# Optimization experiments

Hardware: AMD Instinct MI355X
Metric: run time of the kernel (lower is better)

The kernel has to match this reference:

```python
import jax, jax.numpy as jnp
import numpy as np

N, E, EL = 50000, 150000, 300000   # atoms, bonds(=line-graph nodes), line-graph edges
FN, FE, FX = 128, 128, 64          # atom, bond, angle feature dims (encode_dim)
H, D = 4, 64                        # num_heads, per-head hidden
SLOPE = 0.01                        # torch leaky_relu default


def _leaky(x):
    return jnp.where(x >= 0, x, SLOPE * x)


def _seg_softmax(logits, seg, n):
    # softmax over edges grouped by destination (DGL edge_softmax). logits [E, H]
    m = jax.ops.segment_max(logits, seg, num_segments=n)
    ex = jnp.exp(logits - m[seg])
    s = jax.ops.segment_sum(ex, seg, num_segments=n)
    return ex / s[seg]


def _seg_mean(x, seg, n):
    # mean of incoming edge feats per dst node; empty segments -> 0 (DGL behavior)
    s = jax.ops.segment_sum(x, seg, num_segments=n)
    c = jax.ops.segment_sum(jnp.ones((x.shape[0], 1), x.dtype), seg, num_segments=n)
    return s / jnp.maximum(c, 1.0)


def setup_inputs() -> dict:
    key = jax.random.key(0)
    ks = iter(jax.random.split(key, 40))
    nrm = lambda shape, sc=0.1: jax.random.normal(next(ks), shape, jnp.float32) * sc
    z = lambda n: jnp.zeros((n,), jnp.float32)
    inp = {
        'nfeats': nrm((N, FN), 1.0),
        'efeats': nrm((E, FE), 1.0),
        'xfeats': nrm((EL, FX), 1.0),
        # EGAT layer (atom graph)
        'e_Wni': nrm((H * D, FN)), 'e_Wnj': nrm((H * D, FN)), 'e_Wfij': nrm((H * D, FE)),
        'e_Wnode': nrm((H * D, FN + FE)), 'e_bnode': z(H * D),
        'e_attn': nrm((H, D)), 'e_bias': z(H * D),
        # Path_Complex line-graph branch
        'lg_Wni': nrm((H * D, D)), 'lg_Wnj': nrm((H * D, D)), 'lg_Wfij': nrm((H * D, FX)),
        'lg_Wnode': nrm((H * D, D + FX)), 'lg_bnode': z(H * D),
        'lg_attn': nrm((H, D)), 'lg_bias': z(H * D),
        # Path_Complex graph branch
        'g_Wni': nrm((H * D, D)), 'g_Wnj': nrm((H * D, D)), 'g_Wfij': nrm((H * D, D)),
        'g_Wnode': nrm((H * D, D + D)), 'g_bnode': z(H * D),
        'g_attn': nrm((H, D)), 'g_bias': z(H * D),
        # graph / line-graph connectivity
        'src': jax.random.randint(next(ks), (E,), 0, N, jnp.int32),
        'dst': jax.random.randint(next(ks), (E,), 0, N, jnp.int32),
        'lsrc': jax.random.randint(next(ks), (EL,), 0, E, jnp.int32),
        'ldst': jax.random.randint(next(ks), (EL,), 0, E, jnp.int32),
    }
    return inp


def _forward(nfeats, efeats, xfeats,
             e_Wni, e_Wnj, e_Wfij, e_Wnode, e_bnode, e_attn, e_bias,
             lg_Wni, lg_Wnj, lg_Wfij, lg_Wnode, lg_bnode, lg_attn, lg_bias,
             g_Wni, g_Wnj, g_Wfij, g_Wnode, g_bnode, g_attn, g_bias,
             src, dst, lsrc, ldst):
    # ---- EGAT layer on atom graph ----
    fo = _leaky((nfeats @ e_Wni.T)[src] + (nfeats @ e_Wnj.T)[dst] + efeats @ e_Wfij.T + e_bias)
    fov = fo.reshape(E, H, D)
    e_att = _seg_softmax((fov * e_attn[None]).sum(-1), dst, N)      # [E, H]
    agg = _seg_mean(efeats, dst, N)                                   # [N, FE]
    h = (jnp.concatenate([nfeats, agg], 1) @ e_Wnode.T + e_bnode).reshape(N, H, D)
    h_node = _leaky(jax.ops.segment_sum(h[src] * e_att[:, :, None], dst, num_segments=N)).sum(1)
    f_edge = fov.sum(1)                                               # [E, D]

    # ---- Path_Complex layer: line-graph (bond->angle) branch ----
    lgf = _leaky((f_edge @ lg_Wni.T)[lsrc] + (f_edge @ lg_Wnj.T)[ldst] + xfeats @ lg_Wfij.T + lg_bias)
    lgv = lgf.reshape(EL, H, D)
    a_lg = _seg_softmax((lgv * lg_attn[None]).sum(-1), ldst, E)      # [EL, H]
    aggx = _seg_mean(xfeats, ldst, E)                                 # [E, FX]
    m1 = (jnp.concatenate([f_edge, aggx], 1) @ lg_Wnode.T + lg_bnode).reshape(E, H, D)
    lg_h = _leaky(jax.ops.segment_sum(m1[lsrc] * a_lg[:, :, None], ldst, num_segments=E)).sum(1)

    # ---- Path_Complex layer: graph (atom->bond) branch ----
    gf = _leaky((h_node @ g_Wni.T)[src] + (h_node @ g_Wnj.T)[dst] + f_edge @ g_Wfij.T + g_bias)
    gv = gf.reshape(E, H, D)
    a_g = _seg_softmax((gv * g_attn[None]).sum(-1), dst, N)          # [E, H] -> l_graph ndata 'a'
    node_edge = h_node[src] + h_node[dst]
    m2 = (jnp.concatenate([node_edge, f_edge], 1) @ g_Wnode.T + g_bnode).reshape(E, H, D)
    # u_mul_v on line graph: message = h_out[lsrc] * a[ldst]
    g_h = _leaky(jax.ops.segment_sum(m2[lsrc] * a_g[ldst][:, :, None], ldst, num_segments=E)).sum(1)

    return g_h + lg_h                                                 # [E, D] updated bond feats


def reference(nfeats, efeats, xfeats,
              e_Wni, e_Wnj, e_Wfij, e_Wnode, e_bnode, e_attn, e_bias,
              lg_Wni, lg_Wnj, lg_Wfij, lg_Wnode, lg_bnode, lg_attn, lg_bias,
              g_Wni, g_Wnj, g_Wfij, g_Wnode, g_bnode, g_attn, g_bias,
              src, dst, lsrc, ldst):
    return _forward(nfeats, efeats, xfeats,
                    e_Wni, e_Wnj, e_Wfij, e_Wnode, e_bnode, e_attn, e_bias,
                    lg_Wni, lg_Wnj, lg_Wfij, lg_Wnode, lg_bnode, lg_attn, lg_bias,
                    g_Wni, g_Wnj, g_Wfij, g_Wnode, g_bnode, g_attn, g_bias,
                    src, dst, lsrc, ldst)
```

## Files before the change

### kernel.cpp

```cpp
#include <hip/hip_runtime.h>
#include <hip/hip_bf16.h>
#include <math.h>

typedef __hip_bfloat16 bf16;
typedef short bf16x8 __attribute__((ext_vector_type(8)));
typedef short s16x4 __attribute__((ext_vector_type(4)));
typedef float f32x4 __attribute__((ext_vector_type(4)));

__device__ __forceinline__ float b2f(bf16 x) { return __bfloat162float(x); }
__device__ __forceinline__ bf16  f2b(float x) { return __float2bfloat16(x); }
__device__ __forceinline__ float leaky(float x) { return x >= 0.0f ? x : 0.01f * x; }
__device__ __forceinline__ float sb2f(short s) {
  return __uint_as_float(((unsigned)(unsigned short)s) << 16);
}
__device__ __forceinline__ short f2bs(float x) {
  unsigned u = __float_as_uint(x);
  u += 0x7FFFu + ((u >> 16) & 1u);
  return (short)(u >> 16);
}
__device__ __forceinline__ float ldF(const void* p, size_t i, int f) {
  return f ? ((const float*)p)[i] : b2f(((const bf16*)p)[i]);
}
__device__ __forceinline__ bf16x8 ldA8(const char* row, int k, int f) {
  if (!f) return *(const bf16x8*)(row + (size_t)k * 2);
  const float4* p = (const float4*)(row + (size_t)k * 4);
  float4 a = p[0], b = p[1];
  bf16x8 r;
  r[0] = f2bs(a.x); r[1] = f2bs(a.y); r[2] = f2bs(a.z); r[3] = f2bs(a.w);
  r[4] = f2bs(b.x); r[5] = f2bs(b.y); r[6] = f2bs(b.z); r[7] = f2bs(b.w);
  return r;
}

__global__ void k_detect(const unsigned* __restrict__ w, int* __restrict__ flag) {
  __shared__ int cnt[256];
  unsigned x = w[threadIdx.x];
  unsigned ex = (x >> 7) & 0xFFu;
  cnt[threadIdx.x] = (ex >= 96u && ex <= 144u) ? 1 : 0;
  __syncthreads();
  for (int s = 128; s > 0; s >>= 1) {
    if (threadIdx.x < s) cnt[threadIdx.x] += cnt[threadIdx.x + s];
    __syncthreads();
  }
  if (threadIdx.x == 0) *flag = (cnt[0] < 128) ? 1 : 0;
}

struct WArgs { const void* src[21]; int beg[22]; int len[21]; };
__global__ void k_cvt_all(WArgs wa, bf16* __restrict__ dst, int total,
                          const int* __restrict__ flagp) {
  int f = *flagp;
  for (int i = blockIdx.x * 256 + threadIdx.x; i < total; i += gridDim.x * 256) {
    int t = 0;
    while (t < 20 && i >= wa.beg[t + 1]) ++t;
    int loc = i - wa.beg[t];
    bf16 v = f2b(0.0f);
    if (loc < wa.len[t])
      v = f ? f2b(((const float*)wa.src[t])[loc]) : ((const bf16*)wa.src[t])[loc];
    dst[i] = v;
  }
}

__global__ void k_cvt2(const float* __restrict__ a, bf16* __restrict__ da, size_t na,
                       const float* __restrict__ c, bf16* __restrict__ dc, size_t nc,
                       const int* __restrict__ flagp) {
  if (!*flagp) return;
  size_t tot = (na + nc) >> 2;
  for (size_t i = (size_t)blockIdx.x * 256 + threadIdx.x; i < tot;
       i += (size_t)gridDim.x * 256) {
    size_t j = i << 2;
    const float* s; bf16* d; size_t loc;
    if (j < na) { s = a; d = da; loc = j; }
    else        { s = c; d = dc; loc = j - na; }
    float4 v = *(const float4*)(s + loc);
    s16x4 o; o[0] = f2bs(v.x); o[1] = f2bs(v.y); o[2] = f2bs(v.z); o[3] = f2bs(v.w);
    *(s16x4*)(d + loc) = o;
  }
}

__global__ void k_izero(int* __restrict__ p, int n) {
  int i = blockIdx.x * 256 + threadIdx.x;
  for (; i < n; i += gridDim.x * 256) p[i] = 0;
}

__global__ void k_hist(const int* __restrict__ seg, int* __restrict__ deg, int n) {
  int i = blockIdx.x * 256 + threadIdx.x;
  if (i < n) atomicAdd(&deg[seg[i]], 1);
}

__global__ __launch_bounds__(256)
void k_scan_local(const int* __restrict__ deg, int* __restrict__ rp,
                  int* __restrict__ bsum, int n) {
  __shared__ int sh[256];
  int tid = threadIdx.x;
  int base = blockIdx.x * 4096 + tid * 16;
  int v[16]; int s = 0;
#pragma unroll
  for (int j = 0; j < 16; ++j) { v[j] = (base + j < n) ? deg[base + j] : 0; s += v[j]; }
  sh[tid] = s;
  __syncthreads();
  for (int o = 1; o < 256; o <<= 1) {
    int t = (tid >= o) ? sh[tid - o] : 0;
    __syncthreads();
    sh[tid] += t;
    __syncthreads();
  }
  int run = sh[tid] - s;
#pragma unroll
  for (int j = 0; j < 16; ++j) {
    run += v[j];
    if (base + j < n) rp[base + j + 1] = run;
  }
  if (tid == 255) bsum[blockIdx.x] = sh[255];
  if (blockIdx.x == 0 && tid == 0) rp[0] = 0;
}
__global__ __launch_bounds__(256)
void k_scan_bsum(int* __restrict__ bsum, int nb) {
  __shared__ int sh[256];
  __shared__ int carry;
  int tid = threadIdx.x;
  if (tid == 0) carry = 0;
  __syncthreads();
  for (int base = 0; base < nb; base += 256) {
    int i = base + tid;
    int v = (i < nb) ? bsum[i] : 0;
    sh[tid] = v;
    __syncthreads();
    for (int o = 1; o < 256; o <<= 1) {
      int t = (tid >= o) ? sh[tid - o] : 0;
      __syncthreads();
      sh[tid] += t;
      __syncthreads();
    }
    if (i < nb) bsum[i] = carry + sh[tid] - v;
    int tot = sh[255];
    __syncthreads();
    if (tid == 0) carry += tot;
    __syncthreads();
  }
}
__global__ __launch_bounds__(256)
void k_scan_add(int* __restrict__ rp, const int* __restrict__ bsum, int n) {
  int b = blockIdx.x + 1;
  int ofs = bsum[b];
  int base = b * 4096 + threadIdx.x * 16;
#pragma unroll
  for (int j = 0; j < 16; ++j) {
    int idx = base + j + 1;
    if (idx <= n) rp[idx] += ofs;
  }
}

__global__ void k_slot(const int* __restrict__ seg, const int* __restrict__ rp,
                       int* __restrict__ cur, int* __restrict__ eid,
                       const int* __restrict__ aux1, int* __restrict__ av1,
                       int* __restrict__ pos, int n) {
  int i = blockIdx.x * 256 + threadIdx.x;
  if (i >= n) return;
  int t = seg[i];
  int p = atomicAdd(&cur[t], 1);
  int j = rp[t] + p;
  eid[j] = i;
  if (av1) av1[j] = aux1[i];
  if (pos) pos[i] = j;
}

__global__ void k_gmean(const void* __restrict__ X, const void* __restrict__ Xc, int mode,
                        const int* __restrict__ rp, const int* __restrict__ eid,
                        bf16* __restrict__ out, int n, int width,
                        const int* __restrict__ flagp) {
  int f = (mode == 2) ? *flagp : mode;
  if (Xc && f) { X = Xc; f = 0; }
  int d = threadIdx.x;
  int row = blockIdx.x * blockDim.y + threadIdx.y;
  if (row >= n) return;
  int b = rp[row], e = rp[row + 1];
  float s = 0.0f;
  for (int j = b; j < e; ++j) s += ldF(X, (size_t)eid[j] * width + d, f);
  out[(size_t)row * width + d] = f2b(s / fmaxf((float)(e - b), 1.0f));
}

__global__ __launch_bounds__(256)
void k_mgemm(const void* __restrict__ A0, const void* __restrict__ A0c, int m0mode, int K0,
             const void* __restrict__ A1, int m1mode, int Ktot,
             const bf16* __restrict__ W, int whs, const bf16* __restrict__ bias,
             bf16* __restrict__ C, int cs, int M,
             const int* __restrict__ flagp) {
  int tid = threadIdx.x;
  int w = tid >> 6, lane = tid & 63, l15 = lane & 15, q = lane >> 4;
  int h = blockIdx.y;
  int fl = *flagp;
  int f0 = (m0mode == 2) ? fl : m0mode;
  if (A0c && f0) { A0 = A0c; f0 = 0; }
  int f1 = (m1mode == 2) ? fl : m1mode;
  const bf16* Wh = W + (size_t)h * whs;
  int colofs = h * 64;
  int m0 = blockIdx.x * 64 + w * 16;
  int mA = m0 + l15; if (mA > M - 1) mA = M - 1;
  const char* rowA0 = (const char*)A0 + (size_t)mA * K0 * (f0 ? 4 : 2);
  const char* rowA1 = A1 ? (const char*)A1 + (size_t)mA * (Ktot - K0) * (f1 ? 4 : 2) : nullptr;

  f32x4 acc[4] = {{0,0,0,0},{0,0,0,0},{0,0,0,0},{0,0,0,0}};
  for (int k = q * 8; k < Ktot; k += 32) {
    bf16x8 a;
    if (k < K0) a = ldA8(rowA0, k, f0);
    else        a = ldA8(rowA1, k - K0, f1);
    const bf16* wb = Wh + (size_t)l15 * Ktot + k;
#pragma unroll
    for (int t = 0; t < 4; ++t)
      acc[t] = __builtin_amdgcn_mfma_f32_16x16x32_bf16(
          a, *(const bf16x8*)(wb + (size_t)(t * 16) * Ktot), acc[t], 0, 0, 0);
  }
#pragma unroll
  for (int t = 0; t < 4; ++t) {
    int col = t * 16 + l15;
    float bv = bias ? b2f(bias[colofs + col]) : 0.0f;
#pragma unroll
    for (int r = 0; r < 4; ++r) {
      int m = m0 + q * 4 + r;
      if (m < M) C[(size_t)m * cs + colofs + col] = f2b(acc[t][r] + bv);
    }
  }
}

__global__ __launch_bounds__(256)
void k_mgemm2sw(const void* __restrict__ A, const void* __restrict__ Ac, int mode, int K,
                const bf16* __restrict__ W1, const bf16* __restrict__ W2, int whs,
                int h0, int HB, bf16* __restrict__ C1, bf16* __restrict__ C2, int M,
                const int* __restrict__ flagp) {
  int tid = threadIdx.x;
  int w = tid >> 6, lane = tid & 63, l15 = lane & 15, q = lane >> 4;
  int hy = blockIdx.y;
  int h = h0 + hy;
  int f = (mode == 2) ? *flagp : mode;
  if (Ac && f) { A = Ac; f = 0; }
  const bf16* W1h = W1 + (size_t)h * whs;
  const bf16* W2h = W2 + (size_t)h * whs;
  int cs = HB * 64;
  int m0 = blockIdx.x * 64 + w * 16;
  int mA = m0 + l15; if (mA > M - 1) mA = M - 1;
  const char* rowA = (const char*)A + (size_t)mA * K * (f ? 4 : 2);

  f32x4 a1[4] = {{0,0,0,0},{0,0,0,0},{0,0,0,0},{0,0,0,0}};
  f32x4 a2[4] = {{0,0,0,0},{0,0,0,0},{0,0,0,0},{0,0,0,0}};
  for (int k = q * 8; k < K; k += 32) {
    bf16x8 a = ldA8(rowA, k, f);
    const bf16* w1 = W1h + (size_t)l15 * K + k;
    const bf16* w2 = W2h + (size_t)l15 * K + k;
#pragma unroll
    for (int t = 0; t < 4; ++t) {
      a1[t] = __builtin_amdgcn_mfma_f32_16x16x32_bf16(
          a, *(const bf16x8*)(w1 + (size_t)(t * 16) * K), a1[t], 0, 0, 0);
      a2[t] = __builtin_amdgcn_mfma_f32_16x16x32_bf16(
          a, *(const bf16x8*)(w2 + (size_t)(t * 16) * K), a2[t], 0, 0, 0);
    }
  }
  int ofs = l15 * 4 * HB + hy * 4;
#pragma unroll
  for (int r = 0; r < 4; ++r) {
    int m = m0 + q * 4 + r;
    if (m < M) {
      s16x4 o1, o2;
#pragma unroll
      for (int t = 0; t < 4; ++t) { o1[t] = f2bs(a1[t][r]); o2[t] = f2bs(a2[t][r]); }
      *(s16x4*)(C1 + (size_t)m * cs + ofs) = o1;
      *(s16x4*)(C2 + (size_t)m * cs + ofs) = o2;
    }
  }
}

template<int NK>
__global__ __launch_bounds__(256)
void k_mcomb4sw(const void* __restrict__ A, const void* __restrict__ Ac, int mode,
                const bf16* __restrict__ W, int whs,
                const bf16* __restrict__ bias, const bf16* __restrict__ attn,
                const bf16* __restrict__ G1, const bf16* __restrict__ G2,
                const int* __restrict__ gi, const int* __restrict__ gj,
                const int* __restrict__ posw,
                float* __restrict__ lg4, bf16* __restrict__ fout,
                int M, const int* __restrict__ flagp) {
  constexpr int K = NK * 32;
  int tid = threadIdx.x;
  int w = tid >> 6, lane = tid & 63, l15 = lane & 15, q = lane >> 4;
  int f = (mode == 2) ? *flagp : mode;
  if (Ac && f) { A = Ac; f = 0; }
  int m0 = blockIdx.x * 64 + w * 16;
  int mA = m0 + l15; if (mA > M - 1) mA = M - 1;
  const char* rowA = (const char*)A + (size_t)mA * K * (f ? 4 : 2);
  bf16x8 af[NK];
#pragma unroll
  for (int i = 0; i < NK; ++i) af[i] = ldA8(rowA, q * 8 + 32 * i, f);
  int pIdx[4]; bool okr[4];
  bf16x8 gv1[4][2], gv2[4][2];
#pragma unroll
  for (int r = 0; r < 4; ++r) {
    int m = m0 + q * 4 + r;
    okr[r] = m < M; int mc = okr[r] ? m : M - 1;
    pIdx[r] = posw ? posw[mc] : mc;
    const bf16* p1 = G1 + (size_t)gi[mc] * 256 + l15 * 16;
    const bf16* p2 = G2 + (size_t)gj[mc] * 256 + l15 * 16;
    gv1[r][0] = *(const bf16x8*)p1; gv1[r][1] = *(const bf16x8*)(p1 + 8);
    gv2[r][0] = *(const bf16x8*)p2; gv2[r][1] = *(const bf16x8*)(p2 + 8);
  }
  f32x4 fs[4] = {{0,0,0,0},{0,0,0,0},{0,0,0,0},{0,0,0,0}};
#pragma unroll
  for (int h = 0; h < 4; ++h) {
    const bf16* Wh = W + (size_t)h * whs;
    f32x4 acc[4] = {{0,0,0,0},{0,0,0,0},{0,0,0,0},{0,0,0,0}};
#pragma unroll
    for (int i = 0; i < NK; ++i) {
      const bf16* wb = Wh + (size_t)l15 * K + q * 8 + 32 * i;
#pragma unroll
      for (int t = 0; t < 4; ++t)
        acc[t] = __builtin_amdgcn_mfma_f32_16x16x32_bf16(
            af[i], *(const bf16x8*)(wb + (size_t)(t * 16) * K), acc[t], 0, 0, 0);
    }
    float bv[4], av[4];
#pragma unroll
    for (int t = 0; t < 4; ++t) {
      bv[t] = b2f(bias[h * 64 + t * 16 + l15]);
      av[t] = b2f(attn[h * 64 + t * 16 + l15]);
    }
    float part[4];
#pragma unroll
    for (int r = 0; r < 4; ++r) {
      float p = 0.0f;
#pragma unroll
      for (int t = 0; t < 4; ++t) {
        float v = acc[t][r] + bv[t] + sb2f(gv1[r][h >> 1][(h & 1) * 4 + t])
                                    + sb2f(gv2[r][h >> 1][(h & 1) * 4 + t]);
        v = leaky(v);
        p += v * av[t];
        fs[t][r] += v;
      }
      part[r] = p;
    }
#pragma unroll
    for (int o = 1; o < 16; o <<= 1)
#pragma unroll
      for (int r = 0; r < 4; ++r) part[r] += __shfl_xor(part[r], o, 64);
    if (l15 == 0) {
#pragma unroll
      for (int r = 0; r < 4; ++r)
        if (okr[r]) lg4[(size_t)pIdx[r] * 4 + h] = part[r];
    }
  }
  if (fout) {
#pragma unroll
    for (int t = 0; t < 4; ++t) {
      int col = t * 16 + l15;
#pragma unroll
      for (int r = 0; r < 4; ++r)
        if (okr[r]) fout[(size_t)(m0 + q * 4 + r) * 64 + col] = f2b(fs[t][r]);
    }
  }
}

template<int NK>
__global__ __launch_bounds__(256)
void k_mcomb2h(const void* __restrict__ A, const void* __restrict__ Ac, int mode,
               const bf16* __restrict__ W, int whs, int h0,
               const bf16* __restrict__ bias, const bf16* __restrict__ attn,
               const bf16* __restrict__ G1, const bf16* __restrict__ G2,
               const int* __restrict__ gi, const int* __restrict__ gj,
               const int* __restrict__ posw,
               float* __restrict__ lg4, int M, const int* __restrict__ flagp) {
  constexpr int K = NK * 32;
  int tid = threadIdx.x;
  int w = tid >> 6, lane = tid & 63, l15 = lane & 15, q = lane >> 4;
  int f = (mode == 2) ? *flagp : mode;
  if (Ac && f) { A = Ac; f = 0; }
  int m0 = blockIdx.x * 64 + w * 16;
  int mA = m0 + l15; if (mA > M - 1) mA = M - 1;
  const char* rowA = (const char*)A + (size_t)mA * K * (f ? 4 : 2);
  bf16x8 af[NK];
#pragma unroll
  for (int i = 0; i < NK; ++i) af[i] = ldA8(rowA, q * 8 + 32 * i, f);
  int pIdx[4]; bool okr[4];
  bf16x8 gv1[4], gv2[4];
#pragma unroll
  for (int r = 0; r < 4; ++r) {
    int m = m0 + q * 4 + r;
    okr[r] = m < M; int mc = okr[r] ? m : M - 1;
    pIdx[r] = posw ? posw[mc] : mc;
    gv1[r] = *(const bf16x8*)(G1 + (size_t)gi[mc] * 128 + l15 * 8);
    gv2[r] = *(const bf16x8*)(G2 + (size_t)gj[mc] * 128 + l15 * 8);
  }
#pragma unroll
  for (int hy = 0; hy < 2; ++hy) {
    int h = h0 + hy;
    const bf16* Wh = W + (size_t)h * whs;
    f32x4 acc[4] = {{0,0,0,0},{0,0,0,0},{0,0,0,0},{0,0,0,0}};
#pragma unroll
    for (int i = 0; i < NK; ++i) {
      const bf16* wb = Wh + (size_t)l15 * K + q * 8 + 32 * i;
#pragma unroll
      for (int t = 0; t < 4; ++t)
        acc[t] = __builtin_amdgcn_mfma_f32_16x16x32_bf16(
            af[i], *(const bf16x8*)(wb + (size_t)(t * 16) * K), acc[t], 0, 0, 0);
    }
    float bv[4], av[4];
#pragma unroll
    for (int t = 0; t < 4; ++t) {
      bv[t] = b2f(bias[h * 64 + t * 16 + l15]);
      av[t] = b2f(attn[h * 64 + t * 16 + l15]);
    }
    float part[4];
#pragma unroll
    for (int r = 0; r < 4; ++r) {
      float p = 0.0f;
#pragma unroll
      for (int t = 0; t < 4; ++t) {
        float v = acc[t][r] + bv[t] + sb2f(gv1[r][hy * 4 + t]) + sb2f(gv2[r][hy * 4 + t]);
        p += leaky(v) * av[t];
      }
      part[r] = p;
    }
#pragma unroll
    for (int o = 1; o < 16; o <<= 1)
#pragma unroll
      for (int r = 0; r < 4; ++r) part[r] += __shfl_xor(part[r], o, 64);
    if (l15 == 0) {
#pragma unroll
      for (int r = 0; r < 4; ++r)
        if (okr[r]) lg4[(size_t)pIdx[r] * 4 + h] = part[r];
    }
  }
}

__global__ __launch_bounds__(256)
void k_smax4_csr(float* __restrict__ lg, const int* __restrict__ rp, int n) {
  int tid = blockIdx.x * 256 + threadIdx.x;
  int row = tid >> 2, h = tid & 3;
  if (row >= n) return;
  int b = rp[row], e = rp[row + 1];
  float m = -INFINITY;
  for (int j = b; j < e; ++j) m = fmaxf(m, lg[(size_t)j * 4 + h]);
  float s = 0.0f;
  for (int j = b; j < e; ++j) {
    float ex = expf(lg[(size_t)j * 4 + h] - m);
    lg[(size_t)j * 4 + h] = ex;
    s += ex;
  }
  float inv = 1.0f / s;
  for (int j = b; j < e; ++j) lg[(size_t)j * 4 + h] *= inv;
}
__global__ __launch_bounds__(256)
void k_smax4_eid(float* __restrict__ lg, const int* __restrict__ rp,
                 const int* __restrict__ eid, int n) {
  int tid = blockIdx.x * 256 + threadIdx.x;
  int row = tid >> 2, h = tid & 3;
  if (row >= n) return;
  int b = rp[row], e = rp[row + 1];
  float m = -INFINITY;
  for (int j = b; j < e; ++j) m = fmaxf(m, lg[(size_t)eid[j] * 4 + h]);
  float s = 0.0f;
  for (int j = b; j < e; ++j) {
    float ex = expf(lg[(size_t)eid[j] * 4 + h] - m);
    lg[(size_t)eid[j] * 4 + h] = ex;
    s += ex;
  }
  float inv = 1.0f / s;
  for (int j = b; j < e; ++j) lg[(size_t)eid[j] * 4 + h] *= inv;
}

__global__ __launch_bounds__(256)
void k_ghnode(const bf16* __restrict__ H, const float* __restrict__ lg4c,
              const int* __restrict__ rp, const int* __restrict__ srcv,
              bf16* __restrict__ hnode, int N) {
  int d = threadIdx.x, h = threadIdx.y;
  int n = blockIdx.x;
  int b = rp[n], e = rp[n + 1];
  float s = 0.0f;
  for (int j = b; j < e; ++j)
    s += b2f(H[(size_t)srcv[j] * 256 + h * 64 + d]) * lg4c[(size_t)j * 4 + h];
  float v = leaky(s);
  __shared__ float sh[4][64];
  if (h > 0) sh[h][d] = v;
  __syncthreads();
  if (h == 0)
    hnode[(size_t)n * 64 + d] = f2b(v + sh[1][d] + sh[2][d] + sh[3][d]);
}

__global__ void k_gout2(const bf16* __restrict__ M1, const float* __restrict__ lgE4,
                        int h, const int* __restrict__ rp, const int* __restrict__ lsv,
                        float* __restrict__ out, int E, int first) {
  int d = threadIdx.x;
  int t = blockIdx.x * 4 + threadIdx.y;
  if (t >= E) return;
  int b = rp[t], e = rp[t + 1];
  float s = 0.0f;
  for (int j = b; j < e; ++j)
    s += b2f(M1[(size_t)lsv[j] * 64 + d]) * lgE4[(size_t)j * 4 + h];
  float val = leaky(s);
  if (first) out[(size_t)t * 64 + d] = val;
  else       out[(size_t)t * 64 + d] += val;
}

__global__ void k_gout3(const bf16* __restrict__ M2, const float* __restrict__ lg4n,
                        const int* __restrict__ rp, const int* __restrict__ lsv,
                        float* __restrict__ out, int E, int h) {
  int d = threadIdx.x;
  int t = blockIdx.x * 4 + threadIdx.y;
  if (t >= E) return;
  int b = rp[t], e = rp[t + 1];
  float s = 0.0f;
  for (int j = b; j < e; ++j) s += b2f(M2[(size_t)lsv[j] * 64 + d]);
  float a = lg4n[(size_t)t * 4 + h];
  out[(size_t)t * 64 + d] += leaky(a * s);
}

__global__ void k_addpair(const bf16* __restrict__ hn, const int* __restrict__ src,
                          const int* __restrict__ dst, bf16* __restrict__ ne, int E) {
  int d = threadIdx.x;
  int e = blockIdx.x * 4 + threadIdx.y;
  if (e >= E) return;
  ne[(size_t)e * 64 + d] =
      f2b(b2f(hn[(size_t)src[e] * 64 + d]) + b2f(hn[(size_t)dst[e] * 64 + d]));
}

__global__ void k_cast(void* __restrict__ out, const float* __restrict__ a, size_t n,
                       const int* __restrict__ flagp) {
  int f = *flagp;
  size_t i = (size_t)blockIdx.x * blockDim.x + threadIdx.x;
  size_t st = (size_t)gridDim.x * blockDim.x;
  for (; i < n; i += st) {
    if (f) ((float*)out)[i] = a[i];
    else   ((bf16*)out)[i] = f2b(a[i]);
  }
}

extern "C" void kernel_launch(void* const* d_in, const int* in_sizes, int n_in,
                              void* d_out, int out_size, void* d_ws, size_t ws_size,
                              hipStream_t stream) {
  const int* src  = (const int*)d_in[24];
  const int* dst  = (const int*)d_in[25];
  const int* lsrc = (const int*)d_in[26];
  const int* ldst = (const int*)d_in[27];

  const int N  = in_sizes[0] / 128;
  const int E  = in_sizes[24];
  const int EL = in_sizes[26];
  (void)n_in; (void)out_size; (void)ws_size;

  char* base = (char*)d_ws;
  size_t off = 0;
  auto alloc = [&](size_t bytes) -> char* {
    char* p = base + off;
    off = (off + bytes + 255) & ~(size_t)255;
    return p;
  };
  int* flag = (int*)alloc(256);
  size_t wofs[28]; size_t wtot = 0;
  for (int i = 3; i <= 23; ++i) { wofs[i] = wtot; wtot += (size_t)((in_sizes[i] + 127) & ~127); }
  bf16* WA = (bf16*)alloc(wtot * 2);

  int*   tmpi  = (int*)alloc((size_t)2 * E * 4);
  int*   rpN   = (int*)alloc((size_t)(N + 1) * 4);
  int*   eidN  = (int*)alloc((size_t)E * 4);
  int*   srcv  = (int*)alloc((size_t)E * 4);
  int*   posN  = (int*)alloc((size_t)E * 4);
  int*   rpE   = (int*)alloc((size_t)(E + 1) * 4);
  int*   eidEL = (int*)alloc((size_t)EL * 4);
  int*   lsv   = (int*)alloc((size_t)EL * 4);
  int*   posE  = (int*)alloc((size_t)EL * 4);
  int*   bsum  = (int*)alloc(((size_t)((E > N ? E : N) + 4095) / 4096 + 8) * 4);
  bf16*  fedge = (bf16*)alloc((size_t)E * 64 * 2);
  bf16*  hnode = (bf16*)alloc((size_t)N * 64 * 2);
  float* outacc= (float*)alloc((size_t)E * 64 * 4);
  bf16*  aggB  = (bf16*)alloc((size_t)E * 64 * 2);
  size_t saElems = (size_t)E * 128 > (size_t)N * 256 ? (size_t)E * 128 : (size_t)N * 256;
  bf16*  SA    = (bf16*)alloc(saElems * 2);
  float* logE4 = (float*)alloc((size_t)E * 4 * 4);
  float* logEL4= (float*)alloc((size_t)EL * 4 * 4);
  bf16*  nb    = (bf16*)alloc((size_t)N * 128 * 2);

  bf16* SBo = (bf16*)outacc;
  bf16* xb  = (bf16*)d_out;

  dim3 blk(256);
  const unsigned tN = (N + 63) / 64, tEg = (E + 63) / 64, tELg = (EL + 63) / 64;
  const unsigned gE4 = (E + 3) / 4;
  const unsigned cE = (E + 255) / 256, cEL = (EL + 255) / 256;
  const int nbN = (N + 4095) / 4096, nbE = (E + 4095) / 4096;

  k_detect<<<dim3(1), blk, 0, stream>>>((const unsigned*)d_in[0], flag);
  WArgs wa;
  for (int i = 3; i <= 23; ++i) {
    wa.src[i - 3] = d_in[i];
    wa.beg[i - 3] = (int)wofs[i];
    wa.len[i - 3] = in_sizes[i];
  }
  wa.beg[21] = (int)wtot;
  k_cvt_all<<<dim3(512), blk, 0, stream>>>(wa, WA, (int)wtot, flag);
  k_cvt2<<<dim3(2048), blk, 0, stream>>>(
      (const float*)d_in[0], nb, (size_t)N * 128,
      (const float*)d_in[2], xb, (size_t)EL * 64, flag);

  int* deg = tmpi; int* cur = tmpi + E;
  k_izero<<<dim3(1024), blk, 0, stream>>>(tmpi, 2 * E);
  k_hist<<<dim3(cE), blk, 0, stream>>>(dst, deg, E);
  k_scan_local<<<dim3(nbN), blk, 0, stream>>>(deg, rpN, bsum, N);
  k_scan_bsum<<<dim3(1), blk, 0, stream>>>(bsum, nbN);
  if (nbN > 1) k_scan_add<<<dim3(nbN - 1), blk, 0, stream>>>(rpN, bsum, N);
  k_slot<<<dim3(cE), blk, 0, stream>>>(dst, rpN, cur, eidN, src, srcv, posN, E);
  k_izero<<<dim3(1024), blk, 0, stream>>>(tmpi, 2 * E);
  k_hist<<<dim3(cEL), blk, 0, stream>>>(ldst, deg, EL);
  k_scan_local<<<dim3(nbE), blk, 0, stream>>>(deg, rpE, bsum, E);
  k_scan_bsum<<<dim3(1), blk, 0, stream>>>(bsum, nbE);
  if (nbE > 1) k_scan_add<<<dim3(nbE - 1), blk, 0, stream>>>(rpE, bsum, E);
  k_slot<<<dim3(cEL), blk, 0, stream>>>(ldst, rpE, cur, eidEL, lsrc, lsv, posE, EL);

  k_gmean<<<dim3((N + 1) / 2), dim3(128, 2), 0, stream>>>(d_in[1], nullptr, 2, rpN, eidN,
                                                          aggB, N, 128, flag);
  k_mgemm2sw<<<dim3(tN, 4), blk, 0, stream>>>(d_in[0], nb, 2, 128,
      WA + wofs[3], WA + wofs[4], 8192, 0, 4, SA, SBo, N, flag);
  k_mcomb4sw<4><<<dim3(tEg), blk, 0, stream>>>(d_in[1], nullptr, 2, WA + wofs[5], 8192,
      WA + wofs[9], WA + wofs[8], SA, SBo, src, dst, posN, logE4, fedge, E, flag);
  k_smax4_csr<<<dim3((N * 4 + 255) / 256), blk, 0, stream>>>(logE4, rpN, N);
  k_mgemm<<<dim3(tN, 4), blk, 0, stream>>>(d_in[0], nb, 2, 128, aggB, 0, 256,
      WA + wofs[6], 16384, WA + wofs[7], SA, 256, N, flag);
  k_ghnode<<<dim3(N), dim3(64, 4), 0, stream>>>(SA, logE4, rpN, srcv, hnode, N);

  k_gmean<<<dim3(gE4), dim3(64, 4), 0, stream>>>(d_in[2], xb, 2, rpE, eidEL, aggB, E, 64, flag);
  for (int p = 0; p < 2; ++p) {
    k_mgemm2sw<<<dim3(tEg, 2), blk, 0, stream>>>(fedge, nullptr, 0, 64,
        WA + wofs[10], WA + wofs[11], 4096, 2 * p, 2, SA, SBo, E, flag);
    k_mcomb2h<2><<<dim3(tELg), blk, 0, stream>>>(d_in[2], xb, 2, WA + wofs[12], 4096, 2 * p,
        WA + wofs[16], WA + wofs[15], SA, SBo, lsrc, ldst, posE, logEL4, EL, flag);
  }
  k_smax4_csr<<<dim3((E * 4 + 255) / 256), blk, 0, stream>>>(logEL4, rpE, E);
  for (int h = 0; h < 4; ++h) {
    k_mgemm<<<dim3(tEg, 1), blk, 0, stream>>>(fedge, nullptr, 0, 64, aggB, 0, 128,
        WA + wofs[13] + (size_t)h * 8192, 0, WA + wofs[14] + h * 64,
        SA, 64, E, flag);
    k_gout2<<<dim3(gE4), dim3(64, 4), 0, stream>>>(SA, logEL4, h, rpE, lsv,
                                                   outacc, E, h == 0 ? 1 : 0);
  }

  for (int p = 0; p < 2; ++p) {
    k_mgemm2sw<<<dim3(tN, 2), blk, 0, stream>>>(hnode, nullptr, 0, 64,
        WA + wofs[17], WA + wofs[18], 4096, 2 * p, 2, SA, SA + (size_t)N * 128, N, flag);
    k_mcomb2h<2><<<dim3(tEg), blk, 0, stream>>>(fedge, nullptr, 0, WA + wofs[19], 4096, 2 * p,
        WA + wofs[23], WA + wofs[22], SA, SA + (size_t)N * 128, src, dst, nullptr,
        logE4, E, flag);
  }
  k_smax4_eid<<<dim3((N * 4 + 255) / 256), blk, 0, stream>>>(logE4, rpN, eidN, N);
  k_addpair<<<dim3(gE4), dim3(64, 4), 0, stream>>>(hnode, src, dst, aggB, E);
  for (int h = 0; h < 4; ++h) {
    k_mgemm<<<dim3(tEg, 1), blk, 0, stream>>>(aggB, nullptr, 0, 64, fedge, 0, 128,
        WA + wofs[20] + (size_t)h * 8192, 0, WA + wofs[21] + h * 64,
        SA, 64, E, flag);
    k_gout3<<<dim3(gE4), dim3(64, 4), 0, stream>>>(SA, logE4, rpE, lsv,
                                                   outacc, E, h);
  }

  k_cast<<<dim3(2048), blk, 0, stream>>>(d_out, outacc, (size_t)E * 64, flag);
}
```

Baseline: 1.838 ms.

## Aggregate line-graph inputs before projection, fuse all heads into one GEMM

The graph-branch message (a linear projection of concatenated node-pair and edge features, gathered over line-graph neighbours) is now computed by first summing the raw 128-wide inputs per destination and then applying the projection once. Bias is scaled by in-degree. A single MFMA kernel then processes all four heads with the attention scale and leaky activation fused, replacing four GEMM and gather launches. This removes repeated per-head gathers of projected rows and the intermediate writes, at the cost of aggregating in bf16, which changes rounding.

```diff
diff --git a/kernel.cpp b/kernel.cpp
--- a/kernel.cpp
+++ b/kernel.cpp
@@ -495,17 +495,74 @@
   else       out[(size_t)t * 64 + d] += val;
 }
 
-__global__ void k_gout3(const bf16* __restrict__ M2, const float* __restrict__ lg4n,
-                        const int* __restrict__ rp, const int* __restrict__ lsv,
-                        float* __restrict__ out, int E, int h) {
+__global__ void k_gagg(const bf16* __restrict__ ne, const bf16* __restrict__ fe,
+                       const int* __restrict__ rp, const int* __restrict__ lsv,
+                       bf16* __restrict__ agg, int E) {
   int d = threadIdx.x;
   int t = blockIdx.x * 4 + threadIdx.y;
   if (t >= E) return;
   int b = rp[t], e = rp[t + 1];
-  float s = 0.0f;
-  for (int j = b; j < e; ++j) s += b2f(M2[(size_t)lsv[j] * 64 + d]);
-  float a = lg4n[(size_t)t * 4 + h];
-  out[(size_t)t * 64 + d] += leaky(a * s);
+  float s1 = 0.0f, s2 = 0.0f;
+  for (int j = b; j < e; ++j) {
+    size_t row = (size_t)lsv[j] * 64 + d;
+    s1 += b2f(ne[row]);
+    s2 += b2f(fe[row]);
+  }
+  agg[(size_t)t * 128 + d]      = f2b(s1);
+  agg[(size_t)t * 128 + 64 + d] = f2b(s2);
+}
+
+__global__ __launch_bounds__(256)
+void k_mgemm3(const bf16* __restrict__ A, const bf16* __restrict__ W, int whs,
+              const bf16* __restrict__ bias, const float* __restrict__ lg4n,
+              const int* __restrict__ rp, float* __restrict__ out, int M) {
+  int tid = threadIdx.x;
+  int w = tid >> 6, lane = tid & 63, l15 = lane & 15, q = lane >> 4;
+  int m0 = blockIdx.x * 64 + w * 16;
+  int mA = m0 + l15; if (mA > M - 1) mA = M - 1;
+  const bf16* rowA = A + (size_t)mA * 128;
+  bf16x8 af[4];
+#pragma unroll
+  for (int i = 0; i < 4; ++i) af[i] = *(const bf16x8*)(rowA + q * 8 + 32 * i);
+  bool okr[4]; float degv[4]; float av[4][4];
+#pragma unroll
+  for (int r = 0; r < 4; ++r) {
+    int m = m0 + q * 4 + r;
+    okr[r] = m < M; int mc = okr[r] ? m : M - 1;
+    degv[r] = (float)(rp[mc + 1] - rp[mc]);
+#pragma unroll
+    for (int h = 0; h < 4; ++h) av[r][h] = lg4n[(size_t)mc * 4 + h];
+  }
+  float osum[4][4] = {{0,0,0,0},{0,0,0,0},{0,0,0,0},{0,0,0,0}};
+#pragma unroll
+  for (int h = 0; h < 4; ++h) {
+    const bf16* Wh = W + (size_t)h * whs;
+    f32x4 acc[4] = {{0,0,0,0},{0,0,0,0},{0,0,0,0},{0,0,0,0}};
+#pragma unroll
+    for (int i = 0; i < 4; ++i) {
+      const bf16* wb = Wh + (size_t)l15 * 128 + q * 8 + 32 * i;
+#pragma unroll
+      for (int t = 0; t < 4; ++t)
+        acc[t] = __builtin_amdgcn_mfma_f32_16x16x32_bf16(
+            af[i], *(const bf16x8*)(wb + (size_t)(t * 16) * 128), acc[t], 0, 0, 0);
+    }
+#pragma unroll
+    for (int t = 0; t < 4; ++t) {
+      float bv = b2f(bias[h * 64 + t * 16 + l15]);
+#pragma unroll
+      for (int r = 0; r < 4; ++r)
+        osum[t][r] += leaky(av[r][h] * (acc[t][r] + degv[r] * bv));
+    }
+  }
+#pragma unroll
+  for (int t = 0; t < 4; ++t) {
+    int col = t * 16 + l15;
+#pragma unroll
+    for (int r = 0; r < 4; ++r) {
+      int m = m0 + q * 4 + r;
+      if (m < M) out[(size_t)m * 64 + col] += osum[t][r];
+    }
+  }
 }
 
 __global__ void k_addpair(const bf16* __restrict__ hn, const int* __restrict__ src,
@@ -645,13 +702,9 @@
   }
   k_smax4_eid<<<dim3((N * 4 + 255) / 256), blk, 0, stream>>>(logE4, rpN, eidN, N);
   k_addpair<<<dim3(gE4), dim3(64, 4), 0, stream>>>(hnode, src, dst, aggB, E);
-  for (int h = 0; h < 4; ++h) {
-    k_mgemm<<<dim3(tEg, 1), blk, 0, stream>>>(aggB, nullptr, 0, 64, fedge, 0, 128,
-        WA + wofs[20] + (size_t)h * 8192, 0, WA + wofs[21] + h * 64,
-        SA, 64, E, flag);
-    k_gout3<<<dim3(gE4), dim3(64, 4), 0, stream>>>(SA, logE4, rpE, lsv,
-                                                   outacc, E, h);
-  }
+  k_gagg<<<dim3(gE4), dim3(64, 4), 0, stream>>>(aggB, fedge, rpE, lsv, SA, E);
+  k_mgemm3<<<dim3(tEg), blk, 0, stream>>>(SA, WA + wofs[20], 8192, WA + wofs[21],
+                                          logE4, rpE, outacc, E);
 
   k_cast<<<dim3(2048), blk, 0, stream>>>(d_out, outacc, (size_t)E * 64, flag);
 }
```

Result: faster. 1.639 ms (-10.8%).
